# Kernel tuning notes

Hardware: AMD Instinct MI355X
Metric: run time of the kernel (lower is better)

The kernel has to match this reference:

```python
import jax, jax.numpy as jnp
import numpy as np

N_EMBD = 768
NUM_EXPERTS = 64
EXPERT_WIDTH = 256            # all experts uniform width (expert_sizes=[(64,256)])
TOTAL_WIDTH = NUM_EXPERTS * EXPERT_WIDTH  # 16384
TOP_K = 8


def setup_inputs() -> dict:
    key = jax.random.key(0)
    k1, k2, k3, k4 = jax.random.split(key, 4)
    B, S = 1, 2048
    x = jax.random.normal(k1, (B, S, N_EMBD), dtype=jnp.float32)
    # router: nn.Linear(n_embd, num_experts, bias=False) -> weight [E, n_embd]
    router_w = jax.random.normal(k2, (NUM_EXPERTS, N_EMBD), dtype=jnp.float32) * 0.02
    # trunc_normal(std=0.02) approximated by clipped normal
    w1 = jnp.clip(jax.random.normal(k3, (N_EMBD, TOTAL_WIDTH), dtype=jnp.float32) * 0.02, -0.06, 0.06)
    w2 = jnp.clip(jax.random.normal(k4, (TOTAL_WIDTH, N_EMBD), dtype=jnp.float32) * 0.02, -0.06, 0.06)
    return {"x": x, "router_w": router_w, "w1": w1, "w2": w2}


def reference(x, router_w, w1, w2):
    B, S, D = x.shape
    T = B * S
    x_flat = x.reshape(T, D)

    # Router: sigmoid gating + top-k
    router_logits = x_flat @ router_w.T                      # [T, E]
    router_probs = jax.nn.sigmoid(router_logits.astype(jnp.float32))
    top_k_weights, selected_experts = jax.lax.top_k(router_probs, TOP_K)  # [T, K]
    top_k_weights = top_k_weights / (top_k_weights.sum(axis=-1, keepdims=True) + 1e-20)
    top_k_weights = top_k_weights.astype(x.dtype)

    # Per-token expert combine weights [T, E]: 0 for unselected experts.
    tok_idx = jnp.arange(T)[:, None]
    w_tok = jnp.zeros((T, NUM_EXPERTS), dtype=x.dtype).at[tok_idx, selected_experts].set(top_k_weights)

    # Expert MLP (relu^2 activation), dense-masked equivalent of
    # padded_gather -> grouped GEMM -> padded_scatter.
    h = jnp.square(jax.nn.relu(x_flat @ w1))                 # [T, E*W]
    h = (h.reshape(T, NUM_EXPERTS, EXPERT_WIDTH) * w_tok[:, :, None]).reshape(T, TOTAL_WIDTH)
    output = (h @ w2).reshape(B, S, D)

    # Aux losses
    router_z_loss = jnp.mean(jnp.square(jax.nn.logsumexp(router_logits, axis=-1)))
    tokens_per_expert = jnp.zeros((NUM_EXPERTS,), dtype=jnp.float32).at[selected_experts.reshape(-1)].add(1.0)
    f_i = (tokens_per_expert / tokens_per_expert.sum()).astype(x.dtype)
    p_i = router_probs.mean(axis=0)
    # all expert widths equal -> num_experts * (f_i . p_i)
    load_balance_loss = NUM_EXPERTS * (f_i.astype(jnp.float32) @ p_i)
    # expert_widths_normalized == ones -> mean over tokens of sum of probs
    compute_loss = router_probs.sum(axis=-1).mean()

    return output, router_z_loss, load_balance_loss, compute_loss, f_i
```

## Files before the change

### kernel.cpp

```cpp
#include <hip/hip_runtime.h>
#include <hip/hip_bf16.h>

#define T_TOKENS 2048
#define D_EMBD 768
#define N_EXP 64
#define EW 256
#define TOPK 8
#define TW (N_EXP*EW)
#define PAD_SLOTS 32768
#define SCHED_MAX 128
#define OUT_BASE (2048*768)

typedef __attribute__((ext_vector_type(8))) short bf16x8;
typedef __attribute__((ext_vector_type(4))) float f32x4;

typedef __attribute__((address_space(1))) void GAS;
typedef __attribute__((address_space(3))) void LAS;
#define GLOAD16(g, l) __builtin_amdgcn_global_load_lds((GAS*)(g), (LAS*)(l), 16, 0, 0)

__device__ inline unsigned short f2bu(float f) {
  union { __hip_bfloat16 b; unsigned short u; } cv; cv.b = __float2bfloat16(f); return cv.u;
}
__device__ inline unsigned int pk2(float a, float b) {
  return (unsigned int)f2bu(a) | ((unsigned int)f2bu(b) << 16);
}

__global__ void k_init(int* counts, int* cursor, float* psum, float* scal,
                       float* wgt_slot, int* tok_slot, int* sched_e) {
  int i = blockIdx.x*256 + threadIdx.x;
  if (i < N_EXP) { counts[i] = 0; cursor[i] = 0; psum[i] = 0.f; }
  if (i < 2) scal[i] = 0.f;
  if (i < PAD_SLOTS) { wgt_slot[i] = 0.f; tok_slot[i] = 0; }
  if (i < SCHED_MAX) sched_e[i] = -1;
}

__global__ void k_cvt_x(const float* __restrict__ x, __hip_bfloat16* __restrict__ xb) {
  int i = blockIdx.x*256 + threadIdx.x;
  float4 v = reinterpret_cast<const float4*>(x)[i];
  ushort4 o;
  o.x = f2bu(v.x); o.y = f2bu(v.y); o.z = f2bu(v.z); o.w = f2bu(v.w);
  reinterpret_cast<ushort4*>(xb)[i] = o;
}

__global__ __launch_bounds__(256) void k_logits(const float* __restrict__ x,
                                                const float* __restrict__ rw,
                                                float* __restrict__ lp) {
  __shared__ float rw_s[8][256];
  int tid = threadIdx.x;
  int tg = blockIdx.x, eg = blockIdx.y, kc = blockIdx.z;
  #pragma unroll
  for (int idx = 0; idx < 8; idx++)
    rw_s[idx][tid] = rw[(size_t)(eg*8 + idx)*D_EMBD + kc*256 + tid];
  __syncthreads();
  int tok = tg*256 + tid;
  const float4* x4 = reinterpret_cast<const float4*>(x + (size_t)tok*D_EMBD + kc*256);
  float acc[8];
  #pragma unroll
  for (int e = 0; e < 8; e++) acc[e] = 0.f;
  #pragma unroll 4
  for (int k4 = 0; k4 < 64; k4++) {
    float4 xv = x4[k4];
    #pragma unroll
    for (int e = 0; e < 8; e++)
      acc[e] += xv.x*rw_s[e][k4*4+0] + xv.y*rw_s[e][k4*4+1]
              + xv.z*rw_s[e][k4*4+2] + xv.w*rw_s[e][k4*4+3];
  }
  float* dst = lp + (size_t)kc*T_TOKENS*N_EXP + (size_t)tok*N_EXP + eg*8;
  float4 o0 = {acc[0], acc[1], acc[2], acc[3]};
  float4 o1 = {acc[4], acc[5], acc[6], acc[7]};
  reinterpret_cast<float4*>(dst)[0] = o0;
  reinterpret_cast<float4*>(dst)[1] = o1;
}

__global__ __launch_bounds__(256) void k_router2(const float* __restrict__ lp,
                          int* __restrict__ sel_e, float* __restrict__ sel_w,
                          int* __restrict__ counts, float* __restrict__ psum,
                          float* __restrict__ scal) {
  __shared__ float psum_s[4][64];
  __shared__ int cnt_s[4][64];
  int tid = threadIdx.x, wv = tid >> 6, lane = tid & 63;
  float pacc = 0.f, zacc = 0.f;
  int cacc = 0;
  int tbase = blockIdx.x*8 + wv*2;
  #pragma unroll
  for (int it = 0; it < 2; it++) {
    int t = tbase + it;
    float logit = lp[(size_t)t*N_EXP + lane]
                + lp[(size_t)T_TOKENS*N_EXP + (size_t)t*N_EXP + lane]
                + lp[2*(size_t)T_TOKENS*N_EXP + (size_t)t*N_EXP + lane];
    float prob = 1.f/(1.f + expf(-logit));
    pacc += prob;
    float mx = logit;
    for (int s = 32; s; s >>= 1) mx = fmaxf(mx, __shfl_xor(mx, s, 64));
    float sse = expf(logit - mx);
    for (int s = 32; s; s >>= 1) sse += __shfl_xor(sse, s, 64);
    float lse = mx + logf(sse);
    zacc += lse*lse;
    int rank = 0;
    #pragma unroll
    for (int j = 0; j < 64; j++) {
      float pj = __shfl(prob, j, 64);
      rank += (pj > prob || (pj == prob && j < lane)) ? 1 : 0;
    }
    bool sel = rank < TOPK;
    float sp = sel ? prob : 0.f;
    for (int s = 32; s; s >>= 1) sp += __shfl_xor(sp, s, 64);
    if (sel) {
      sel_e[t*TOPK + rank] = lane;
      sel_w[t*TOPK + rank] = prob / (sp + 1e-20f);
      cacc++;
    }
  }
  psum_s[wv][lane] = pacc;
  cnt_s[wv][lane] = cacc;
  if (lane == 0) atomicAdd(&scal[0], zacc);
  __syncthreads();
  if (tid < 64) {
    float p = psum_s[0][tid] + psum_s[1][tid] + psum_s[2][tid] + psum_s[3][tid];
    int c = cnt_s[0][tid] + cnt_s[1][tid] + cnt_s[2][tid] + cnt_s[3][tid];
    atomicAdd(&psum[tid], p);
    atomicAdd(&counts[tid], c);
  }
}

__global__ void k_schedule(const int* __restrict__ counts, int* __restrict__ offsets,
                           int* __restrict__ sched_e, int* __restrict__ sched_r0) {
  int e = threadIdx.x;
  int c = counts[e];
  int tiles = (c + 255) >> 8;
  int padded = tiles << 8;
  int ip = padded;
  for (int s = 1; s < 64; s <<= 1) { int v = __shfl_up(ip, s, 64); if (e >= s) ip += v; }
  int rowoff = ip - padded;
  offsets[e] = rowoff;
  int it = tiles;
  for (int s = 1; s < 64; s <<= 1) { int v = __shfl_up(it, s, 64); if (e >= s) it += v; }
  int rank = it - tiles;
  for (int i = 0; i < tiles; i++) {
    sched_e[rank + i] = e;
    sched_r0[rank + i] = rowoff + i*256;
  }
}

__global__ void k_assign(const int* __restrict__ sel_e, const float* __restrict__ sel_w,
                         const int* __restrict__ offsets, int* __restrict__ cursor,
                         int* __restrict__ tok_slot, float* __restrict__ wgt_slot,
                         int* __restrict__ slot_tk) {
  int i = blockIdx.x*256 + threadIdx.x;
  int e = sel_e[i];
  int pos = atomicAdd(&cursor[e], 1);
  int slot = offsets[e] + pos;
  tok_slot[slot] = i >> 3;
  wgt_slot[slot] = sel_w[i];
  slot_tk[i] = slot;
}

template<int MODE>
__global__ __launch_bounds__(512) void k_moe_gemm(
    const void* __restrict__ Asrc, const float* __restrict__ Bsrc,
    const int* __restrict__ sched_e, const int* __restrict__ sched_r0,
    const int* __restrict__ tok_slot, const float* __restrict__ wgt_slot,
    __hip_bfloat16* __restrict__ outp) {
  constexpr int NS   = (MODE == 1) ? 12 : 4;
  constexpr int BSTR = (MODE == 1) ? TW : D_EMBD;
  __shared__ __hip_bfloat16 As[2][256*64];
  __shared__ __hip_bfloat16 Bs[2][128*64];
  int tid = threadIdx.x;
  int nch = blockIdx.y;
  int cp = tid & 63, ko = tid >> 6;
  int arl = tid >> 3, akc = tid & 7;
  int aoff = (akc ^ (arl & 7))*8;
  int wv = tid >> 6, lane = tid & 63;
  int wm = wv >> 1, wn = wv & 1;
  int l15 = lane & 15, l4 = lane >> 4;

  int p = blockIdx.x;
  int e = sched_e[p];
  if (e < 0) return;
  int r0 = sched_r0[p];

  size_t brow0 = (MODE == 1) ? 0 : (size_t)e*EW;
  int bcol = (MODE == 1) ? (e*EW + nch*128) : nch*128;

  size_t abase[4];
  #pragma unroll
  for (int i = 0; i < 4; i++) {
    if (MODE == 1) abase[i] = (size_t)tok_slot[r0 + i*64 + arl] * D_EMBD;
    else           abase[i] = (size_t)(r0 + i*64 + arl) * EW;
  }

  float2 bv[8];

  auto B_LD = [&](int k0) {
    const float* rp = Bsrc + (brow0 + k0 + ko*8)*BSTR + bcol + cp*2;
    #pragma unroll
    for (int r = 0; r < 8; r++)
      bv[r] = *reinterpret_cast<const float2*>(rp + (size_t)r*BSTR);
  };
  auto B_WR = [&](int bsel) {
    char* bs = (char*)&Bs[bsel][0];
    #pragma unroll
    for (int c = 0; c < 2; c++) {
      int n = cp*2 + c;
      int ch = ko ^ ((n & 7) ^ ((n >> 3) & 7));
      float v0 = c ? bv[0].y : bv[0].x, v1 = c ? bv[1].y : bv[1].x;
      float v2 = c ? bv[2].y : bv[2].x, v3 = c ? bv[3].y : bv[3].x;
      float v4 = c ? bv[4].y : bv[4].x, v5 = c ? bv[5].y : bv[5].x;
      float v6 = c ? bv[6].y : bv[6].x, v7 = c ? bv[7].y : bv[7].x;
      uint4 o = { pk2(v0, v1), pk2(v2, v3), pk2(v4, v5), pk2(v6, v7) };
      *reinterpret_cast<uint4*>(bs + n*128 + ch*16) = o;
    }
  };
  auto A_ST = [&](int bsel, int k0) {
    const __hip_bfloat16* ab = (const __hip_bfloat16*)Asrc;
    #pragma unroll
    for (int i = 0; i < 4; i++)
      GLOAD16(ab + abase[i] + k0 + aoff, &As[bsel][0] + (i*512 + tid)*8);
  };

  f32x4 acc[4][4];
  f32x4 z = {0.f, 0.f, 0.f, 0.f};
  #pragma unroll
  for (int m = 0; m < 4; m++)
    #pragma unroll
    for (int n = 0; n < 4; n++) acc[m][n] = z;

  auto COMPUTE = [&](int bsel) {
    const char* asC = (const char*)&As[bsel][0];
    const char* bsC = (const char*)&Bs[bsel][0];
    bf16x8 af[4][2], bq[4][2];
    #pragma unroll
    for (int m = 0; m < 4; m++) {
      int ra = wm*64 + m*16 + l15;
      #pragma unroll
      for (int kk = 0; kk < 2; kk++)
        af[m][kk] = *reinterpret_cast<const bf16x8*>(
            asC + ra*128 + (((kk*4 + l4) ^ (ra & 7)) << 4));
    }
    #pragma unroll
    for (int n = 0; n < 4; n++) {
      int rb = wn*64 + n*16 + l15;
      int Sb = (rb & 7) ^ ((rb >> 3) & 7);
      #pragma unroll
      for (int kk = 0; kk < 2; kk++)
        bq[n][kk] = *reinterpret_cast<const bf16x8*>(
            bsC + rb*128 + (((kk*4 + l4) ^ Sb) << 4));
    }
    #pragma unroll
    for (int kk = 0; kk < 2; kk++)
      #pragma unroll
      for (int m = 0; m < 4; m++)
        #pragma unroll
        for (int n = 0; n < 4; n++)
          acc[m][n] = __builtin_amdgcn_mfma_f32_16x16x32_bf16(af[m][kk], bq[n][kk], acc[m][n], 0, 0, 0);
  };

  A_ST(0, 0);
  B_LD(0);
  B_WR(0);
  asm volatile("s_waitcnt vmcnt(0)" ::: "memory");
  __syncthreads();

  int cur = 0;
  for (int step = 0; step < NS; step++) {
    bool more = (step + 1 < NS);
    if (more) { A_ST(cur ^ 1, (step + 1)*64); B_LD((step + 1)*64); }
    COMPUTE(cur);
    if (more) B_WR(cur ^ 1);
    asm volatile("s_waitcnt vmcnt(0)" ::: "memory");
    __syncthreads();
    cur ^= 1;
  }

  if (MODE == 1) {
    #pragma unroll
    for (int m = 0; m < 4; m++)
      #pragma unroll
      for (int j = 0; j < 4; j++) {
        int r = r0 + wm*64 + m*16 + l4*4 + j;
        float wg = wgt_slot[r];
        #pragma unroll
        for (int n = 0; n < 4; n++) {
          int col = nch*128 + wn*64 + n*16 + l15;
          float v = fmaxf(acc[m][n][j], 0.f);
          outp[(size_t)r*EW + col] = __float2bfloat16(v*v*wg);
        }
      }
  } else {
    #pragma unroll
    for (int m = 0; m < 4; m++)
      #pragma unroll
      for (int j = 0; j < 4; j++) {
        int r = r0 + wm*64 + m*16 + l4*4 + j;
        #pragma unroll
        for (int n = 0; n < 4; n++) {
          int col = nch*128 + wn*64 + n*16 + l15;
          outp[(size_t)r*D_EMBD + col] = __float2bfloat16(acc[m][n][j]);
        }
      }
  }
}

__global__ void k_combine(const __hip_bfloat16* __restrict__ y, const int* __restrict__ slot_tk,
                          float* __restrict__ out) {
  __shared__ int s[TOPK];
  int t = blockIdx.x, tid = threadIdx.x;
  if (tid < TOPK) s[tid] = slot_tk[t*TOPK + tid];
  __syncthreads();
  if (tid < 192) {
    int c = tid*4;
    float a0 = 0.f, a1 = 0.f, a2 = 0.f, a3 = 0.f;
    #pragma unroll
    for (int k = 0; k < TOPK; k++) {
      ushort4 v = *reinterpret_cast<const ushort4*>(&y[(size_t)s[k]*D_EMBD + c]);
      union { unsigned int u; float f; } f0, f1, f2, f3;
      f0.u = ((unsigned int)v.x) << 16;
      f1.u = ((unsigned int)v.y) << 16;
      f2.u = ((unsigned int)v.z) << 16;
      f3.u = ((unsigned int)v.w) << 16;
      a0 += f0.f; a1 += f1.f; a2 += f2.f; a3 += f3.f;
    }
    float4 o = {a0, a1, a2, a3};
    *reinterpret_cast<float4*>(&out[(size_t)t*D_EMBD + c]) = o;
  }
}

__global__ void k_finalize(const int* __restrict__ counts, const float* __restrict__ psum,
                           const float* __restrict__ scal, float* __restrict__ out) {
  __shared__ float part[N_EXP], ptot[N_EXP];
  int e = threadIdx.x;
  float f = (float)counts[e] / 16384.f;
  float p = psum[e] / 2048.f;
  part[e] = f * p;
  ptot[e] = p;
  out[OUT_BASE + 3 + e] = f;
  __syncthreads();
  if (e == 0) {
    float s = 0.f, q = 0.f;
    for (int i = 0; i < N_EXP; i++) { s += part[i]; q += ptot[i]; }
    out[OUT_BASE + 0] = scal[0] / 2048.f;
    out[OUT_BASE + 1] = 64.f * s;
    out[OUT_BASE + 2] = q;
  }
}

extern "C" void kernel_launch(void* const* d_in, const int* in_sizes, int n_in,
                              void* d_out, int out_size, void* d_ws, size_t ws_size,
                              hipStream_t stream) {
  const float* x  = (const float*)d_in[0];
  const float* rw = (const float*)d_in[1];
  const float* w1 = (const float*)d_in[2];
  const float* w2 = (const float*)d_in[3];
  float* out = (float*)d_out;
  char* ws = (char*)d_ws;

  size_t o = 0;
  auto alloc = [&](size_t b) { size_t r = o; o += (b + 255) & ~(size_t)255; return r; };
  __hip_bfloat16* xb    = (__hip_bfloat16*)(ws + alloc(2048UL*768*2));
  __hip_bfloat16* hprm  = (__hip_bfloat16*)(ws + alloc((size_t)PAD_SLOTS*256*2));
  __hip_bfloat16* yprm  = (__hip_bfloat16*)(ws + alloc((size_t)PAD_SLOTS*768*2));
  float* lp      = (float*)(ws + alloc(3UL*2048*64*4));
  int*   sel_e   = (int*)  (ws + alloc(16384UL*4));
  float* sel_w   = (float*)(ws + alloc(16384UL*4));
  int*   slot_tk = (int*)  (ws + alloc(16384UL*4));
  int*   tokslot = (int*)  (ws + alloc((size_t)PAD_SLOTS*4));
  float* wgtslot = (float*)(ws + alloc((size_t)PAD_SLOTS*4));
  int*   counts  = (int*)  (ws + alloc(256));
  int*   cursor  = (int*)  (ws + alloc(256));
  float* psum    = (float*)(ws + alloc(256));
  float* scal    = (float*)(ws + alloc(256));
  int*   offsets = (int*)  (ws + alloc(256));
  int*   sch_e   = (int*)  (ws + alloc(SCHED_MAX*4));
  int*   sch_r0  = (int*)  (ws + alloc(SCHED_MAX*4));

  k_init<<<128, 256, 0, stream>>>(counts, cursor, psum, scal, wgtslot, tokslot, sch_e);
  k_cvt_x<<<1536, 256, 0, stream>>>(x, xb);
  k_logits<<<dim3(8, 8, 3), 256, 0, stream>>>(x, rw, lp);
  k_router2<<<256, 256, 0, stream>>>(lp, sel_e, sel_w, counts, psum, scal);
  k_schedule<<<1, 64, 0, stream>>>(counts, offsets, sch_e, sch_r0);
  k_assign<<<64, 256, 0, stream>>>(sel_e, sel_w, offsets, cursor, tokslot, wgtslot, slot_tk);
  k_moe_gemm<1><<<dim3(SCHED_MAX, 2), 512, 0, stream>>>((const void*)xb, w1, sch_e, sch_r0, tokslot, wgtslot, hprm);
  k_moe_gemm<2><<<dim3(SCHED_MAX, 6), 512, 0, stream>>>((const void*)hprm, w2, sch_e, sch_r0, tokslot, wgtslot, yprm);
  k_combine<<<2048, 256, 0, stream>>>(yprm, slot_tk, out);
  k_finalize<<<1, 64, 0, stream>>>(counts, psum, scal, out);
}
```

Measured before the change: 145.0 us.

## Repack weights to bf16 K-panels and shrink MoE GEMM tiles to 128 rows

Adds two kernels that convert w1 and w2 from fp32 into bf16 per-expert, per-K-chunk transposed panels. The grouped GEMMs can then stage B tiles with direct global-to-LDS loads instead of fp32 register loads, conversion and swizzled LDS writes. The M tile is also halved to 128 rows with 256-thread blocks and the schedule padded to 128-row tiles, which cuts padding waste and increases block count. The cost is an extra full pass over both weight matrices on every call (about 100 MB read and 50 MB written) to repack them.

Result: slower. 164.7 us (+13.6%).

```diff
diff --git a/kernel.cpp b/kernel.cpp
--- a/kernel.cpp
+++ b/kernel.cpp
@@ -7,8 +7,8 @@
 #define EW 256
 #define TOPK 8
 #define TW (N_EXP*EW)
-#define PAD_SLOTS 32768
-#define SCHED_MAX 128
+#define PAD_SLOTS 24576
+#define SCHED_MAX 192
 #define OUT_BASE (2048*768)
 
 typedef __attribute__((ext_vector_type(8))) short bf16x8;
@@ -20,9 +20,6 @@
 
 __device__ inline unsigned short f2bu(float f) {
   union { __hip_bfloat16 b; unsigned short u; } cv; cv.b = __float2bfloat16(f); return cv.u;
-}
-__device__ inline unsigned int pk2(float a, float b) {
-  return (unsigned int)f2bu(a) | ((unsigned int)f2bu(b) << 16);
 }
 
 __global__ void k_init(int* counts, int* cursor, float* psum, float* scal,
@@ -40,6 +37,56 @@
   ushort4 o;
   o.x = f2bu(v.x); o.y = f2bu(v.y); o.z = f2bu(v.z); o.w = f2bu(v.w);
   reinterpret_cast<ushort4*>(xb)[i] = o;
+}
+
+__global__ __launch_bounds__(256) void k_repack1(const float* __restrict__ w1,
+                                                 __hip_bfloat16* __restrict__ w1p) {
+  __shared__ unsigned short t[256][72];
+  int e = blockIdx.x & 63, kc = blockIdx.x >> 6;
+  int tid = threadIdx.x;
+  int r = tid >> 2, cq = tid & 3;
+  const float4* src = reinterpret_cast<const float4*>(
+      w1 + (size_t)(kc*64 + r)*TW + e*256 + cq*64);
+  #pragma unroll
+  for (int i = 0; i < 16; i++) {
+    float4 v = src[i];
+    int c = cq*64 + i*4;
+    t[c+0][r] = f2bu(v.x); t[c+1][r] = f2bu(v.y);
+    t[c+2][r] = f2bu(v.z); t[c+3][r] = f2bu(v.w);
+  }
+  __syncthreads();
+  int n = tid;
+  __hip_bfloat16* dst = w1p + (size_t)(e*12 + kc)*16384 + n*64;
+  const uint4* row = reinterpret_cast<const uint4*>(&t[n][0]);
+  #pragma unroll
+  for (int j = 0; j < 8; j++)
+    reinterpret_cast<uint4*>(dst)[j] = row[j];
+}
+
+__global__ __launch_bounds__(256) void k_repack2(const float* __restrict__ w2,
+                                                 __hip_bfloat16* __restrict__ w2p) {
+  __shared__ unsigned short t[768][72];
+  int e = blockIdx.x >> 2, kc = blockIdx.x & 3;
+  int tid = threadIdx.x;
+  const float* base = w2 + (size_t)(e*256 + kc*64)*D_EMBD;
+  for (int it = 0; it < 48; it++) {
+    int idx = it*256 + tid;
+    int r = idx / 192, c4 = idx - r*192;
+    float4 v = *reinterpret_cast<const float4*>(base + (size_t)r*D_EMBD + c4*4);
+    int c = c4*4;
+    t[c+0][r] = f2bu(v.x); t[c+1][r] = f2bu(v.y);
+    t[c+2][r] = f2bu(v.z); t[c+3][r] = f2bu(v.w);
+  }
+  __syncthreads();
+  #pragma unroll
+  for (int pass = 0; pass < 3; pass++) {
+    int n = pass*256 + tid;
+    __hip_bfloat16* dst = w2p + (size_t)(e*4 + kc)*49152 + n*64;
+    const uint4* row = reinterpret_cast<const uint4*>(&t[n][0]);
+    #pragma unroll
+    for (int j = 0; j < 8; j++)
+      reinterpret_cast<uint4*>(dst)[j] = row[j];
+  }
 }
 
 __global__ __launch_bounds__(256) void k_logits(const float* __restrict__ x,
@@ -127,8 +174,8 @@
                            int* __restrict__ sched_e, int* __restrict__ sched_r0) {
   int e = threadIdx.x;
   int c = counts[e];
-  int tiles = (c + 255) >> 8;
-  int padded = tiles << 8;
+  int tiles = (c + 127) >> 7;
+  int padded = tiles << 7;
   int ip = padded;
   for (int s = 1; s < 64; s <<= 1) { int v = __shfl_up(ip, s, 64); if (e >= s) ip += v; }
   int rowoff = ip - padded;
@@ -138,7 +185,7 @@
   int rank = it - tiles;
   for (int i = 0; i < tiles; i++) {
     sched_e[rank + i] = e;
-    sched_r0[rank + i] = rowoff + i*256;
+    sched_r0[rank + i] = rowoff + i*128;
   }
 }
 
@@ -156,20 +203,19 @@
 }
 
 template<int MODE>
-__global__ __launch_bounds__(512) void k_moe_gemm(
-    const void* __restrict__ Asrc, const float* __restrict__ Bsrc,
+__global__ __launch_bounds__(256) void k_moe_gemm(
+    const __hip_bfloat16* __restrict__ Ab, const __hip_bfloat16* __restrict__ Bp,
     const int* __restrict__ sched_e, const int* __restrict__ sched_r0,
     const int* __restrict__ tok_slot, const float* __restrict__ wgt_slot,
     __hip_bfloat16* __restrict__ outp) {
-  constexpr int NS   = (MODE == 1) ? 12 : 4;
-  constexpr int BSTR = (MODE == 1) ? TW : D_EMBD;
-  __shared__ __hip_bfloat16 As[2][256*64];
+  constexpr int NS    = (MODE == 1) ? 12 : 4;
+  constexpr int NKC   = (MODE == 1) ? 12 : 4;
+  constexpr int PANEL = (MODE == 1) ? 16384 : 49152;
+  __shared__ __hip_bfloat16 As[2][128*64];
   __shared__ __hip_bfloat16 Bs[2][128*64];
   int tid = threadIdx.x;
   int nch = blockIdx.y;
-  int cp = tid & 63, ko = tid >> 6;
-  int arl = tid >> 3, akc = tid & 7;
-  int aoff = (akc ^ (arl & 7))*8;
+  int arow = tid >> 3, akc = tid & 7;
   int wv = tid >> 6, lane = tid & 63;
   int wm = wv >> 1, wn = wv & 1;
   int l15 = lane & 15, l4 = lane >> 4;
@@ -179,43 +225,26 @@
   if (e < 0) return;
   int r0 = sched_r0[p];
 
-  size_t brow0 = (MODE == 1) ? 0 : (size_t)e*EW;
-  int bcol = (MODE == 1) ? (e*EW + nch*128) : nch*128;
+  size_t pb0 = (size_t)(e*NKC)*PANEL + (nch*128)*64;
 
   size_t abase[4];
+  int aswz[4];
   #pragma unroll
   for (int i = 0; i < 4; i++) {
-    if (MODE == 1) abase[i] = (size_t)tok_slot[r0 + i*64 + arl] * D_EMBD;
-    else           abase[i] = (size_t)(r0 + i*64 + arl) * EW;
-  }
-
-  float2 bv[8];
-
-  auto B_LD = [&](int k0) {
-    const float* rp = Bsrc + (brow0 + k0 + ko*8)*BSTR + bcol + cp*2;
-    #pragma unroll
-    for (int r = 0; r < 8; r++)
-      bv[r] = *reinterpret_cast<const float2*>(rp + (size_t)r*BSTR);
-  };
-  auto B_WR = [&](int bsel) {
-    char* bs = (char*)&Bs[bsel][0];
-    #pragma unroll
-    for (int c = 0; c < 2; c++) {
-      int n = cp*2 + c;
-      int ch = ko ^ ((n & 7) ^ ((n >> 3) & 7));
-      float v0 = c ? bv[0].y : bv[0].x, v1 = c ? bv[1].y : bv[1].x;
-      float v2 = c ? bv[2].y : bv[2].x, v3 = c ? bv[3].y : bv[3].x;
-      float v4 = c ? bv[4].y : bv[4].x, v5 = c ? bv[5].y : bv[5].x;
-      float v6 = c ? bv[6].y : bv[6].x, v7 = c ? bv[7].y : bv[7].x;
-      uint4 o = { pk2(v0, v1), pk2(v2, v3), pk2(v4, v5), pk2(v6, v7) };
-      *reinterpret_cast<uint4*>(bs + n*128 + ch*16) = o;
-    }
-  };
-  auto A_ST = [&](int bsel, int k0) {
-    const __hip_bfloat16* ab = (const __hip_bfloat16*)Asrc;
-    #pragma unroll
-    for (int i = 0; i < 4; i++)
-      GLOAD16(ab + abase[i] + k0 + aoff, &As[bsel][0] + (i*512 + tid)*8);
+    int row = i*32 + arow;
+    if (MODE == 1) abase[i] = (size_t)tok_slot[r0 + row] * D_EMBD;
+    else           abase[i] = (size_t)(r0 + row) * EW;
+    aswz[i] = (akc ^ (row & 7))*8;
+  }
+
+  auto STAGE = [&](int bsel, int step) {
+    int k0 = step*64;
+    size_t pb = pb0 + (size_t)step*PANEL;
+    #pragma unroll
+    for (int i = 0; i < 4; i++) {
+      GLOAD16(Ab + abase[i] + k0 + aswz[i], &As[bsel][0] + (i*256 + tid)*8);
+      GLOAD16(Bp + pb + (i*32 + arow)*64 + aswz[i], &Bs[bsel][0] + (i*256 + tid)*8);
+    }
   };
 
   f32x4 acc[4][4];
@@ -240,11 +269,10 @@
     #pragma unroll
     for (int n = 0; n < 4; n++) {
       int rb = wn*64 + n*16 + l15;
-      int Sb = (rb & 7) ^ ((rb >> 3) & 7);
       #pragma unroll
       for (int kk = 0; kk < 2; kk++)
         bq[n][kk] = *reinterpret_cast<const bf16x8*>(
-            bsC + rb*128 + (((kk*4 + l4) ^ Sb) << 4));
+            bsC + rb*128 + (((kk*4 + l4) ^ (rb & 7)) << 4));
     }
     #pragma unroll
     for (int kk = 0; kk < 2; kk++)
@@ -255,18 +283,15 @@
           acc[m][n] = __builtin_amdgcn_mfma_f32_16x16x32_bf16(af[m][kk], bq[n][kk], acc[m][n], 0, 0, 0);
   };
 
-  A_ST(0, 0);
-  B_LD(0);
-  B_WR(0);
+  STAGE(0, 0);
   asm volatile("s_waitcnt vmcnt(0)" ::: "memory");
   __syncthreads();
 
   int cur = 0;
   for (int step = 0; step < NS; step++) {
     bool more = (step + 1 < NS);
-    if (more) { A_ST(cur ^ 1, (step + 1)*64); B_LD((step + 1)*64); }
+    if (more) STAGE(cur ^ 1, step + 1);
     COMPUTE(cur);
-    if (more) B_WR(cur ^ 1);
     asm volatile("s_waitcnt vmcnt(0)" ::: "memory");
     __syncthreads();
     cur ^= 1;
@@ -356,9 +381,11 @@
 
   size_t o = 0;
   auto alloc = [&](size_t b) { size_t r = o; o += (b + 255) & ~(size_t)255; return r; };
-  __hip_bfloat16* xb    = (__hip_bfloat16*)(ws + alloc(2048UL*768*2));
-  __hip_bfloat16* hprm  = (__hip_bfloat16*)(ws + alloc((size_t)PAD_SLOTS*256*2));
-  __hip_bfloat16* yprm  = (__hip_bfloat16*)(ws + alloc((size_t)PAD_SLOTS*768*2));
+  __hip_bfloat16* xb   = (__hip_bfloat16*)(ws + alloc(2048UL*768*2));
+  __hip_bfloat16* w1p  = (__hip_bfloat16*)(ws + alloc(768UL*16384*2));
+  __hip_bfloat16* w2p  = (__hip_bfloat16*)(ws + alloc(16384UL*768*2));
+  __hip_bfloat16* hprm = (__hip_bfloat16*)(ws + alloc((size_t)PAD_SLOTS*256*2));
+  __hip_bfloat16* yprm = (__hip_bfloat16*)(ws + alloc((size_t)PAD_SLOTS*768*2));
   float* lp      = (float*)(ws + alloc(3UL*2048*64*4));
   int*   sel_e   = (int*)  (ws + alloc(16384UL*4));
   float* sel_w   = (float*)(ws + alloc(16384UL*4));
@@ -373,14 +400,16 @@
   int*   sch_e   = (int*)  (ws + alloc(SCHED_MAX*4));
   int*   sch_r0  = (int*)  (ws + alloc(SCHED_MAX*4));
 
-  k_init<<<128, 256, 0, stream>>>(counts, cursor, psum, scal, wgtslot, tokslot, sch_e);
+  k_init<<<96, 256, 0, stream>>>(counts, cursor, psum, scal, wgtslot, tokslot, sch_e);
   k_cvt_x<<<1536, 256, 0, stream>>>(x, xb);
+  k_repack1<<<768, 256, 0, stream>>>(w1, w1p);
+  k_repack2<<<256, 256, 0, stream>>>(w2, w2p);
   k_logits<<<dim3(8, 8, 3), 256, 0, stream>>>(x, rw, lp);
   k_router2<<<256, 256, 0, stream>>>(lp, sel_e, sel_w, counts, psum, scal);
   k_schedule<<<1, 64, 0, stream>>>(counts, offsets, sch_e, sch_r0);
   k_assign<<<64, 256, 0, stream>>>(sel_e, sel_w, offsets, cursor, tokslot, wgtslot, slot_tk);
-  k_moe_gemm<1><<<dim3(SCHED_MAX, 2), 512, 0, stream>>>((const void*)xb, w1, sch_e, sch_r0, tokslot, wgtslot, hprm);
-  k_moe_gemm<2><<<dim3(SCHED_MAX, 6), 512, 0, stream>>>((const void*)hprm, w2, sch_e, sch_r0, tokslot, wgtslot, yprm);
+  k_moe_gemm<1><<<dim3(SCHED_MAX, 2), 256, 0, stream>>>(xb, w1p, sch_e, sch_r0, tokslot, wgtslot, hprm);
+  k_moe_gemm<2><<<dim3(SCHED_MAX, 6), 256, 0, stream>>>(hprm, w2p, sch_e, sch_r0, tokslot, wgtslot, yprm);
   k_combine<<<2048, 256, 0, stream>>>(yprm, slot_tk, out);
   k_finalize<<<1, 64, 0, stream>>>(counts, psum, scal, out);
 }
```
